# Kernel tuning notes

Measured on AMD Instinct MI355X. Metric: run time of the kernel, lower is better.

Reference implementation:

```python
import jax, jax.numpy as jnp
import numpy as np

N, H, W, C, K = 8, 512, 512, 3, 5
PAD = K // 2  # odd square kernel, 'same' zero padding


def setup_inputs() -> dict:
    key = jax.random.key(0)
    k1, k2 = jax.random.split(key)
    input_data = jax.random.normal(k1, (N, H, W, C), dtype=jnp.float32)
    # per-sample, per-pixel unshared kernels: (N, H, W, K*K)
    weights = jax.random.normal(k2, (N, H, W, K * K), dtype=jnp.float32) * 0.1
    return {"input_data": input_data, "weights": weights}


def reference(input_data, weights):
    # Local (untied) depthwise conv: out[n,h,w,c] =
    #   sum_{dh,dw} in[n, h+dh-P, w+dw-P, c] * weights[n, h, w, dh*K+dw]
    # Weight is shared across channels (no channel dim in weights).
    x = jnp.pad(input_data, ((0, 0), (PAD, PAD), (PAD, PAD), (0, 0)))
    out = jnp.zeros_like(input_data)
    for k in range(K * K):  # fixed small loop over kernel taps
        dh, dw = k // K, k % K
        out = out + x[:, dh:dh + H, dw:dw + W, :] * weights[..., k:k + 1]
    return out
```

## Files before the change

### kernel.cpp

```cpp
#include <hip/hip_runtime.h>

#define NN 8
#define HH 512
#define WW 512
#define CC 3
#define KK 5
#define PADP 2
#define WROWF (WW * CC)
#define NBLOCKS (NN * HH * WW / 128)

typedef float f4a __attribute__((ext_vector_type(4), aligned(4)));

struct Row { f4a L0, L1, L2, L3; };

__device__ __forceinline__ void load_row(const float* rb, Row& r) {
    r.L0 = *(const f4a*)(rb);
    r.L1 = *(const f4a*)(rb + 4);
    r.L2 = *(const f4a*)(rb + 8);
    r.L3 = *(const f4a*)(rb + 11);
}

__device__ __forceinline__ void fma_row(const Row& r, const float* wp,
                                        float& a0, float& a1, float& a2) {
    const float w0 = wp[0], w1 = wp[1], w2 = wp[2], w3 = wp[3], w4 = wp[4];
    a0 = fmaf(r.L0[0], w0, a0); a1 = fmaf(r.L0[1], w0, a1); a2 = fmaf(r.L0[2], w0, a2);
    a0 = fmaf(r.L0[3], w1, a0); a1 = fmaf(r.L1[0], w1, a1); a2 = fmaf(r.L1[1], w1, a2);
    a0 = fmaf(r.L1[2], w2, a0); a1 = fmaf(r.L1[3], w2, a1); a2 = fmaf(r.L2[0], w2, a2);
    a0 = fmaf(r.L2[1], w3, a0); a1 = fmaf(r.L2[2], w3, a1); a2 = fmaf(r.L2[3], w3, a2);
    a0 = fmaf(r.L3[1], w4, a0); a1 = fmaf(r.L3[2], w4, a1); a2 = fmaf(r.L3[3], w4, a2);
}

#define GLDS16(gp, lp) __builtin_amdgcn_global_load_lds( \
    (const __attribute__((address_space(1))) void*)(gp), \
    (__attribute__((address_space(3))) void*)(lp), 16, 0, 0)
#define GLDS4(gp, lp) __builtin_amdgcn_global_load_lds( \
    (const __attribute__((address_space(1))) void*)(gp), \
    (__attribute__((address_space(3))) void*)(lp), 4, 0, 0)

__global__ __launch_bounds__(64, 3) void conv_local_kernel(
    const float* __restrict__ in,
    const float* __restrict__ wt,
    float* __restrict__ out)
{
    __shared__ float w_lds[2 * 64 * KK * KK];

    const int lane = threadIdx.x;
    const int b    = ((blockIdx.x & 7) << 11) | (blockIdx.x >> 3);
    const int wseg = b & 7;
    const int hp   = (b >> 3) & 255;
    const int n    = b >> 11;
    const int w0   = wseg << 6;
    const int h0   = hp << 1;

    const long pix0 = ((long)(n * HH + h0)) * WW + w0;
    const long pix1 = pix0 + WW;
    const float* inb = in + (size_t)n * (HH * WW * CC);

    {
        const char* s0 = (const char*)(wt + pix0 * (KK * KK));
        const char* s1 = (const char*)(wt + pix1 * (KK * KK));
#pragma unroll
        for (int it = 0; it < 6; ++it)
            GLDS16(s0 + it * 1024 + lane * 16, &w_lds[it * 256]);
        GLDS4(s0 + 6144 + lane * 4, &w_lds[1536]);
#pragma unroll
        for (int it = 0; it < 6; ++it)
            GLDS16(s1 + it * 1024 + lane * 16, &w_lds[1600 + it * 256]);
        GLDS4(s1 + 6144 + lane * 4, &w_lds[1600 + 1536]);
    }

    const float* wp0 = &w_lds[lane * (KK * KK)];
    const float* wp1 = &w_lds[1600 + lane * (KK * KK)];

    const bool fast = (w0 != 0) && (w0 != WW - 64) && (h0 >= PADP) && (h0 <= HH - 4);

    if (fast) {
        const float* rb = inb + ((long)(h0 - PADP) * WW + (w0 + lane - PADP)) * CC;
        Row R0, R1, R2, R3, R4, R5;
        load_row(rb,             R0);
        load_row(rb + 1 * WROWF, R1);
        load_row(rb + 2 * WROWF, R2);
        load_row(rb + 3 * WROWF, R3);
        load_row(rb + 4 * WROWF, R4);
        load_row(rb + 5 * WROWF, R5);
        asm volatile("s_waitcnt vmcnt(0)" ::: "memory");
        __builtin_amdgcn_sched_barrier(0);

        float a0 = 0.f, a1 = 0.f, a2 = 0.f;
        float c0 = 0.f, c1 = 0.f, c2 = 0.f;

        fma_row(R0, wp0 + 0,  a0, a1, a2);
        fma_row(R1, wp0 + 5,  a0, a1, a2);
        fma_row(R1, wp1 + 0,  c0, c1, c2);
        fma_row(R2, wp0 + 10, a0, a1, a2);
        fma_row(R2, wp1 + 5,  c0, c1, c2);
        fma_row(R3, wp0 + 15, a0, a1, a2);
        fma_row(R3, wp1 + 10, c0, c1, c2);
        fma_row(R4, wp0 + 20, a0, a1, a2);
        fma_row(R4, wp1 + 15, c0, c1, c2);
        fma_row(R5, wp1 + 20, c0, c1, c2);

        float* o0 = out + (pix0 + lane) * CC;
        o0[0] = a0; o0[1] = a1; o0[2] = a2;
        float* o1 = out + (pix1 + lane) * CC;
        o1[0] = c0; o1[1] = c1; o1[2] = c2;
    } else {
        asm volatile("s_waitcnt vmcnt(0)" ::: "memory");
        __builtin_amdgcn_sched_barrier(0);
#pragma unroll
        for (int px = 0; px < 2; ++px) {
            const int hh = h0 + px;
            const int w  = w0 + lane;
            const float* wp = px ? wp1 : wp0;
            float a0 = 0.f, a1 = 0.f, a2 = 0.f;
#pragma unroll
            for (int dh = 0; dh < KK; ++dh) {
                const int ih = hh + dh - PADP;
                const bool rok = ((unsigned)ih < (unsigned)HH);
#pragma unroll
                for (int dw = 0; dw < KK; ++dw) {
                    const int iw = w + dw - PADP;
                    const bool ok = rok && ((unsigned)iw < (unsigned)WW);
                    const float* p = inb + ((long)(ih * WW + iw)) * CC;
                    float v0 = ok ? p[0] : 0.f;
                    float v1 = ok ? p[1] : 0.f;
                    float v2 = ok ? p[2] : 0.f;
                    const float wv = wp[dh * KK + dw];
                    a0 = fmaf(v0, wv, a0);
                    a1 = fmaf(v1, wv, a1);
                    a2 = fmaf(v2, wv, a2);
                }
            }
            float* o = out + (((long)(n * HH + hh)) * WW + w) * CC;
            o[0] = a0; o[1] = a1; o[2] = a2;
        }
    }
}

extern "C" void kernel_launch(void* const* d_in, const int* in_sizes, int n_in,
                              void* d_out, int out_size, void* d_ws, size_t ws_size,
                              hipStream_t stream) {
    const float* in = (const float*)d_in[0];
    const float* wt = (const float*)d_in[1];
    float* out = (float*)d_out;

    conv_local_kernel<<<NBLOCKS, 64, 0, stream>>>(in, wt, out);
}
```

Measured before the change: 58.38 us.

## Process four width segments per block in a serial loop with fewer blocks

The grid shrinks from 16384 to 4096 single-wave blocks, and each block loops over four 64-pixel width segments of a row pair, reusing its LDS weight buffers. The launch-bound occupancy hint rises from 3 to 4 waves. The aim is to cut per-block launch and setup overhead. The cost is that each wave now runs its segments one after another: it waits on LDS and vector memory before every FMA phase, and nothing overlaps across iterations, so the GPU has less latency hiding.

```diff
diff --git a/kernel.cpp b/kernel.cpp
--- a/kernel.cpp
+++ b/kernel.cpp
@@ -7,7 +7,7 @@
 #define KK 5
 #define PADP 2
 #define WROWF (WW * CC)
-#define NBLOCKS (NN * HH * WW / 128)
+#define NBLOCKS 4096
 
 typedef float f4a __attribute__((ext_vector_type(4), aligned(4)));
 
@@ -37,102 +37,110 @@
     (const __attribute__((address_space(1))) void*)(gp), \
     (__attribute__((address_space(3))) void*)(lp), 4, 0, 0)
 
-__global__ __launch_bounds__(64, 3) void conv_local_kernel(
+__global__ __launch_bounds__(64, 4) void conv_local_kernel(
     const float* __restrict__ in,
     const float* __restrict__ wt,
     float* __restrict__ out)
 {
-    __shared__ float w_lds[2 * 64 * KK * KK];
+    __shared__ float wldsA[64 * KK * KK];
+    __shared__ float wldsB[64 * KK * KK];
 
     const int lane = threadIdx.x;
-    const int b    = ((blockIdx.x & 7) << 11) | (blockIdx.x >> 3);
-    const int wseg = b & 7;
-    const int hp   = (b >> 3) & 255;
-    const int n    = b >> 11;
-    const int w0   = wseg << 6;
+    const int b    = ((blockIdx.x & 7) << 9) | (blockIdx.x >> 3);
+    const int n    = b >> 9;
+    const int rem  = b & 511;
+    const int hp   = rem >> 1;
+    const int half = rem & 1;
     const int h0   = hp << 1;
+    const int nHH  = n * HH;
 
-    const long pix0 = ((long)(n * HH + h0)) * WW + w0;
-    const long pix1 = pix0 + WW;
-    const float* inb = in + (size_t)n * (HH * WW * CC);
+    const float* inb  = in + (size_t)n * (HH * WW * CC);
+    const bool  rowok = (hp >= 1) && (hp <= 254);
 
-    {
-        const char* s0 = (const char*)(wt + pix0 * (KK * KK));
-        const char* s1 = (const char*)(wt + pix1 * (KK * KK));
+#pragma unroll 1
+    for (int j = 0; j < 4; ++j) {
+        const int  w0 = (((half << 2) | j)) << 6;
+        const long p0 = (long)(nHH + h0) * WW + w0;
+        const long p1 = p0 + WW;
+
+        asm volatile("s_waitcnt lgkmcnt(0)" ::: "memory");
+
+        {
+            const char* s0 = (const char*)(wt + p0 * (KK * KK));
+            const char* s1 = (const char*)(wt + p1 * (KK * KK));
 #pragma unroll
-        for (int it = 0; it < 6; ++it)
-            GLDS16(s0 + it * 1024 + lane * 16, &w_lds[it * 256]);
-        GLDS4(s0 + 6144 + lane * 4, &w_lds[1536]);
+            for (int it = 0; it < 6; ++it)
+                GLDS16(s0 + it * 1024 + lane * 16, wldsA + it * 256);
+            GLDS4(s0 + 6144 + lane * 4, wldsA + 1536);
 #pragma unroll
-        for (int it = 0; it < 6; ++it)
-            GLDS16(s1 + it * 1024 + lane * 16, &w_lds[1600 + it * 256]);
-        GLDS4(s1 + 6144 + lane * 4, &w_lds[1600 + 1536]);
-    }
+            for (int it = 0; it < 6; ++it)
+                GLDS16(s1 + it * 1024 + lane * 16, wldsB + it * 256);
+            GLDS4(s1 + 6144 + lane * 4, wldsB + 1536);
+        }
 
-    const float* wp0 = &w_lds[lane * (KK * KK)];
-    const float* wp1 = &w_lds[1600 + lane * (KK * KK)];
+        const float* wp0 = &wldsA[lane * (KK * KK)];
+        const float* wp1 = &wldsB[lane * (KK * KK)];
+        const bool fast = rowok && (w0 != 0) && (w0 != WW - 64);
 
-    const bool fast = (w0 != 0) && (w0 != WW - 64) && (h0 >= PADP) && (h0 <= HH - 4);
+        if (fast) {
+            const float* rb = inb + ((long)(h0 - PADP) * WW + (w0 + lane - PADP)) * CC;
+            Row R0, R1, R2, R3, R4, R5;
+            load_row(rb + 0 * WROWF, R0);
+            load_row(rb + 1 * WROWF, R1);
+            load_row(rb + 2 * WROWF, R2);
+            load_row(rb + 3 * WROWF, R3);
+            load_row(rb + 4 * WROWF, R4);
+            load_row(rb + 5 * WROWF, R5);
+            asm volatile("s_waitcnt vmcnt(0)" ::: "memory");
+            __builtin_amdgcn_sched_barrier(0);
 
-    if (fast) {
-        const float* rb = inb + ((long)(h0 - PADP) * WW + (w0 + lane - PADP)) * CC;
-        Row R0, R1, R2, R3, R4, R5;
-        load_row(rb,             R0);
-        load_row(rb + 1 * WROWF, R1);
-        load_row(rb + 2 * WROWF, R2);
-        load_row(rb + 3 * WROWF, R3);
-        load_row(rb + 4 * WROWF, R4);
-        load_row(rb + 5 * WROWF, R5);
-        asm volatile("s_waitcnt vmcnt(0)" ::: "memory");
-        __builtin_amdgcn_sched_barrier(0);
+            float a0 = 0.f, a1 = 0.f, a2 = 0.f;
+            float c0 = 0.f, c1 = 0.f, c2 = 0.f;
+            fma_row(R0, wp0 + 0,  a0, a1, a2);
+            fma_row(R1, wp0 + 5,  a0, a1, a2);
+            fma_row(R1, wp1 + 0,  c0, c1, c2);
+            fma_row(R2, wp0 + 10, a0, a1, a2);
+            fma_row(R2, wp1 + 5,  c0, c1, c2);
+            fma_row(R3, wp0 + 15, a0, a1, a2);
+            fma_row(R3, wp1 + 10, c0, c1, c2);
+            fma_row(R4, wp0 + 20, a0, a1, a2);
+            fma_row(R4, wp1 + 15, c0, c1, c2);
+            fma_row(R5, wp1 + 20, c0, c1, c2);
 
-        float a0 = 0.f, a1 = 0.f, a2 = 0.f;
-        float c0 = 0.f, c1 = 0.f, c2 = 0.f;
-
-        fma_row(R0, wp0 + 0,  a0, a1, a2);
-        fma_row(R1, wp0 + 5,  a0, a1, a2);
-        fma_row(R1, wp1 + 0,  c0, c1, c2);
-        fma_row(R2, wp0 + 10, a0, a1, a2);
-        fma_row(R2, wp1 + 5,  c0, c1, c2);
-        fma_row(R3, wp0 + 15, a0, a1, a2);
-        fma_row(R3, wp1 + 10, c0, c1, c2);
-        fma_row(R4, wp0 + 20, a0, a1, a2);
-        fma_row(R4, wp1 + 15, c0, c1, c2);
-        fma_row(R5, wp1 + 20, c0, c1, c2);
-
-        float* o0 = out + (pix0 + lane) * CC;
-        o0[0] = a0; o0[1] = a1; o0[2] = a2;
-        float* o1 = out + (pix1 + lane) * CC;
-        o1[0] = c0; o1[1] = c1; o1[2] = c2;
-    } else {
-        asm volatile("s_waitcnt vmcnt(0)" ::: "memory");
-        __builtin_amdgcn_sched_barrier(0);
+            float* o0 = out + (p0 + lane) * CC;
+            o0[0] = a0; o0[1] = a1; o0[2] = a2;
+            float* o1 = out + (p1 + lane) * CC;
+            o1[0] = c0; o1[1] = c1; o1[2] = c2;
+        } else {
+            asm volatile("s_waitcnt vmcnt(0)" ::: "memory");
+            __builtin_amdgcn_sched_barrier(0);
 #pragma unroll
-        for (int px = 0; px < 2; ++px) {
-            const int hh = h0 + px;
-            const int w  = w0 + lane;
-            const float* wp = px ? wp1 : wp0;
-            float a0 = 0.f, a1 = 0.f, a2 = 0.f;
+            for (int px = 0; px < 2; ++px) {
+                const int hh = h0 + px;
+                const int w  = w0 + lane;
+                const float* wp = px ? wp1 : wp0;
+                float a0 = 0.f, a1 = 0.f, a2 = 0.f;
 #pragma unroll
-            for (int dh = 0; dh < KK; ++dh) {
-                const int ih = hh + dh - PADP;
-                const bool rok = ((unsigned)ih < (unsigned)HH);
+                for (int dh = 0; dh < KK; ++dh) {
+                    const int ih = hh + dh - PADP;
+                    const bool rok = ((unsigned)ih < (unsigned)HH);
 #pragma unroll
-                for (int dw = 0; dw < KK; ++dw) {
-                    const int iw = w + dw - PADP;
-                    const bool ok = rok && ((unsigned)iw < (unsigned)WW);
-                    const float* p = inb + ((long)(ih * WW + iw)) * CC;
-                    float v0 = ok ? p[0] : 0.f;
-                    float v1 = ok ? p[1] : 0.f;
-                    float v2 = ok ? p[2] : 0.f;
-                    const float wv = wp[dh * KK + dw];
-                    a0 = fmaf(v0, wv, a0);
-                    a1 = fmaf(v1, wv, a1);
-                    a2 = fmaf(v2, wv, a2);
+                    for (int dw = 0; dw < KK; ++dw) {
+                        const int iw = w + dw - PADP;
+                        const bool ok = rok && ((unsigned)iw < (unsigned)WW);
+                        const float* p = inb + ((long)(ih * WW + iw)) * CC;
+                        float v0 = ok ? p[0] : 0.f;
+                        float v1 = ok ? p[1] : 0.f;
+                        float v2 = ok ? p[2] : 0.f;
+                        const float wv = wp[dh * KK + dw];
+                        a0 = fmaf(v0, wv, a0);
+                        a1 = fmaf(v1, wv, a1);
+                        a2 = fmaf(v2, wv, a2);
+                    }
                 }
+                float* o = out + ((long)(nHH + hh) * WW + w) * CC;
+                o[0] = a0; o[1] = a1; o[2] = a2;
             }
-            float* o = out + (((long)(n * HH + hh)) * WW + w) * CC;
-            o[0] = a0; o[1] = a1; o[2] = a2;
         }
     }
 }
```

Result: faster. 56.39 us (median of 2 runs) (-3.4%).
